# Kernel optimization log

Hardware: AMD Instinct MI355X
Metric: run time of the kernel (lower is better)

## Reference

```python
import jax, jax.numpy as jnp
import numpy as np

B, T1, T2, D, H = 16, 512, 64, 768, 12
E = D // H  # head dim


def _proj(x, W, b):
    # x: [B,T,D], W: [6,D,D], b: [6,D] -> [6,B,H,T,E], scaled by E**-0.25 (applied to q,k,v alike, per source)
    t = x.shape[1]
    p = jnp.einsum('btd,kdf->kbtf', x, W) + b[:, None, None, :]
    p = p.reshape(6, B, t, H, E).transpose(0, 1, 3, 2, 4)
    return p * (E ** -0.25)


def setup_inputs() -> dict:
    key = jax.random.key(0)
    ks = jax.random.split(key, 12)
    s = 0.02
    return {
        'feats': jax.random.normal(ks[0], (B, T1, D), jnp.float32),
        'inps': jax.random.normal(ks[1], (B, T2, D), jnp.float32),
        'att_mask': jax.random.randint(ks[2], (B, 1, 1, T1 + T2), 0, 2).astype(bool),
        'W_f': s * jax.random.normal(ks[3], (6, D, D), jnp.float32),
        'b_f': s * jax.random.normal(ks[4], (6, D), jnp.float32),
        'W_i': s * jax.random.normal(ks[5], (6, D, D), jnp.float32),
        'b_i': s * jax.random.normal(ks[6], (6, D), jnp.float32),
        'Wu_v': s * jax.random.normal(ks[7], (D, D), jnp.float32),
        'bu_v': s * jax.random.normal(ks[8], (D,), jnp.float32),
        'Wu_l': s * jax.random.normal(ks[9], (D, D), jnp.float32),
        'bu_l': s * jax.random.normal(ks[10], (D,), jnp.float32),
    }


def reference(feats, inps, att_mask, W_f, b_f, W_i, b_i, Wu_v, bu_v, Wu_l, bu_l):
    NEG = jnp.float32(-1e9)
    # projections from feats: [keys_v_v, queries_v_v, values_v_v, queries_l_v, keys_v_l, values_v_l]
    k_vv, q_vv, v_vv, q_lv, k_vl, v_vl = _proj(feats, W_f, b_f)
    # projections from inps: [keys_l_v, values_l_v, queries_v_l, queries_l_l, keys_l_l, values_l_l]
    k_lv, v_lv, q_vl, q_ll, k_ll, v_ll = _proj(inps, W_i, b_i)

    # visual stream: two distinct queries over the two key blocks, joint softmax over t1+t2
    dot_vv = jnp.einsum('bhqe,bhke->bhqk', q_vv, k_vv)   # [B,H,T1,T1]
    dot_lv = jnp.einsum('bhqe,bhke->bhqk', q_lv, k_lv)   # [B,H,T1,T2]
    att_v = jnp.concatenate([dot_vv, dot_lv], axis=-1)    # [B,H,T1,T1+T2]
    att_v = jax.nn.softmax(jnp.where(att_mask, NEG, att_v), axis=-1)
    vals_v = jnp.concatenate([v_vv, v_lv], axis=2)        # [B,H,T1+T2,E]
    out_v = jnp.einsum('bhqk,bhke->bhqe', att_v, vals_v)
    out_v = out_v.transpose(0, 2, 1, 3).reshape(B, T1, D)
    out_v = out_v @ Wu_v + bu_v

    # language stream
    dot_vl = jnp.einsum('bhqe,bhke->bhqk', q_vl, k_vl)    # [B,H,T2,T1]
    dot_ll = jnp.einsum('bhqe,bhke->bhqk', q_ll, k_ll)    # [B,H,T2,T2]
    att_l = jnp.concatenate([dot_vl, dot_ll], axis=-1)    # [B,H,T2,T1+T2]
    att_l = jax.nn.softmax(jnp.where(att_mask, NEG, att_l), axis=-1)
    vals_l = jnp.concatenate([v_vl, v_ll], axis=2)        # [B,H,T1+T2,E]
    out_l = jnp.einsum('bhqk,bhke->bhqe', att_l, vals_l)
    out_l = out_l.transpose(0, 2, 1, 3).reshape(B, T2, D)
    out_l = out_l @ Wu_l + bu_l

    return (out_v, out_l)
```

## Files before the change

### kernel.cpp

```cpp
#include <hip/hip_runtime.h>
#include <stdint.h>

#define BB 16
#define T1C 512
#define T2C 64
#define DC 768
#define HC 12
#define EC 64
#define SC 576
#define QSCALE 0.35355339059327379f

typedef __attribute__((ext_vector_type(8))) short bf16x8;
typedef __attribute__((ext_vector_type(4))) float f32x4;

__device__ __forceinline__ uint16_t f2b(float f) {
    union { float f; uint32_t i; } v; v.f = f;
    return (uint16_t)((v.i + 0x7fffu + ((v.i >> 16) & 1u)) >> 16);
}
__device__ __forceinline__ uint16_t f2bfast(float f) {
    union { float f; uint32_t i; } v; v.f = f;
    return (uint16_t)((v.i + 0x8000u) >> 16);
}
__device__ __forceinline__ uint32_t pk2(float a, float b) {
    return (uint32_t)f2b(a) | ((uint32_t)f2b(b) << 16);
}

__device__ __forceinline__ void gll16(const void* g, void* l) {
    __builtin_amdgcn_global_load_lds(
        (const __attribute__((address_space(1))) uint32_t*)(uintptr_t)g,
        (__attribute__((address_space(3))) uint32_t*)(uintptr_t)l, 16, 0, 0);
}

__global__ void detect(const uint32_t* __restrict__ mw, int* __restrict__ flags) {
    __shared__ int aW, aB, aL;
    if (threadIdx.x == 0) { aW = 0; aB = 0; aL = 0; }
    __syncthreads();
    int lW = 0, lB = 0, lL = 0;
    for (int i = threadIdx.x; i < 2304; i += 256) {
        uint32_t w = mw[i];
        if (w > 1u) lW = 1;
        if (((w) & 0xffu) > 1u || ((w >> 8) & 0xffu) > 1u ||
            ((w >> 16) & 0xffu) > 1u || ((w >> 24) & 0xffu) > 1u) lB = 1;
        if ((w & 0xffffu) > 1u) lL = 1;
    }
    if (lW) atomicOr(&aW, 1);
    if (lB) atomicOr(&aB, 1);
    if (lL) atomicOr(&aL, 1);
    __syncthreads();
    if (threadIdx.x == 0)
        flags[0] = (!aW) ? 0 : ((!aB) ? 1 : (aL ? 2 : 0));
}

__global__ __launch_bounds__(256) void wtrans(
    const float* __restrict__ Wf, const float* __restrict__ Wi,
    const float* __restrict__ Wuv, const float* __restrict__ Wul,
    uint16_t* __restrict__ Wt)
{
    __shared__ float tile[32][33];
    const int z = blockIdx.z;
    const float* src = (z < 6)  ? Wf + (size_t)z * DC * DC
                     : (z < 12) ? Wi + (size_t)(z - 6) * DC * DC
                     : (z == 12 ? Wuv : Wul);
    uint16_t* dst = Wt + (size_t)z * DC * DC;
    const int tx = threadIdx.x & 31, ty = threadIdx.x >> 5;
    const int k0 = blockIdx.x * 32, f0 = blockIdx.y * 32;
#pragma unroll
    for (int r = 0; r < 4; r++)
        tile[ty + r * 8][tx] = src[(size_t)(k0 + ty + r * 8) * DC + f0 + tx];
    __syncthreads();
#pragma unroll
    for (int r = 0; r < 4; r++)
        dst[(size_t)(f0 + ty + r * 8) * DC + k0 + tx] = f2b(tile[tx][ty + r * 8]);
}

__global__ __launch_bounds__(256) void xswz(
    const float* __restrict__ Xf, const float* __restrict__ Xi,
    uint16_t* __restrict__ Of, uint16_t* __restrict__ Oi)
{
    const int nf = BB * T1C * DC / 8;
    const int ni = BB * T2C * DC / 8;
    int t = blockIdx.x * 256 + threadIdx.x;
    const float* src; uint16_t* dst; int cc;
    if (t < nf) { src = Xf; dst = Of; cc = t; }
    else        { cc = t - nf; if (cc >= ni) return; src = Xi; dst = Oi; }
    int rlid = cc & 15;
    int t2 = cc >> 4;
    int qd = t2 & 3;
    int t3 = t2 >> 2;
    int kt = t3 % 24;
    int p  = t3 / 24;
    const float* sp = src + (size_t)(p * 16 + rlid) * DC + kt * 32 + qd * 8;
    float4 a = *(const float4*)sp;
    float4 b = *(const float4*)(sp + 4);
    uint4 o;
    o.x = pk2(a.x, a.y); o.y = pk2(a.z, a.w);
    o.z = pk2(b.x, b.y); o.w = pk2(b.z, b.w);
    *(uint4*)(dst + (size_t)cc * 8) = o;
}

#define BSTR 76

__global__ __launch_bounds__(256, 4) void gemm_proj_mfma(
    const uint16_t* __restrict__ Xsf, const uint16_t* __restrict__ Xsi,
    const uint16_t* __restrict__ Wt,
    const float* __restrict__ b_f, const float* __restrict__ b_i,
    uint16_t* __restrict__ Pf, uint16_t* __restrict__ Pi)
{
    __shared__ union {
        uint16_t B[2][128 * 32];
        uint16_t bounce[4][16 * BSTR];
    } sm;
    const int tid = threadIdx.x;
    const int w = tid >> 6, l = tid & 63;
    const bool isf = (blockIdx.x < 64);
    const int mx = isf ? blockIdx.x : blockIdx.x - 64;
    const int m0 = mx * 128;
    const int T  = isf ? T1C : T2C;
    const uint16_t* Xs = isf ? Xsf : Xsi;
    const float* bias  = isf ? b_f : b_i;
    uint16_t* P        = isf ? Pf : Pi;
    const int vmask    = isf ? 0x24 : 0x22;
    const int k6 = blockIdx.y / 6, nt = blockIdx.y % 6;
    const int n0 = nt * 128;
    const uint16_t* Bsrc = Wt + (size_t)((isf ? 0 : 6) + k6) * DC * DC;

    const int lid = l & 15, qd = l >> 4;
    const int wm = w >> 1, wn = w & 1;
    const int br = l >> 2, bk = (l & 3) * 8;
    const int p0 = mx * 8 + wm * 4;
    const int c0 = w * 2;

    f32x4 acc[4][4] = {};

#pragma unroll
    for (int n = 0; n < 2; ++n)
        gll16(Bsrc + (size_t)(n0 + (c0 + n) * 16 + br) * DC + bk, &sm.B[0][(c0 + n) * 512]);

    for (int kt = 0; kt < DC / 32; ++kt) {
        uint16_t* Bcur = sm.B[kt & 1];
        uint16_t* Bnxt = sm.B[(kt + 1) & 1];
        bf16x8 af[4];
#pragma unroll
        for (int i = 0; i < 4; i++)
            af[i] = *(const bf16x8*)(Xs + ((size_t)((p0 + i) * 24 + kt) * 64 + l) * 8);
        __builtin_amdgcn_s_barrier();
        __builtin_amdgcn_sched_barrier(0);
        if (kt < 23) {
#pragma unroll
            for (int n = 0; n < 2; ++n)
                gll16(Bsrc + (size_t)(n0 + (c0 + n) * 16 + br) * DC + (kt + 1) * 32 + bk,
                      &Bnxt[(c0 + n) * 512]);
            asm volatile("s_waitcnt vmcnt(2)" ::: "memory");
        } else {
            asm volatile("s_waitcnt vmcnt(0)" ::: "memory");
        }
        __builtin_amdgcn_sched_barrier(0);
        __builtin_amdgcn_s_barrier();
        __builtin_amdgcn_sched_barrier(0);
        bf16x8 bf[4];
#pragma unroll
        for (int j = 0; j < 4; j++)
            bf[j] = *(const bf16x8*)&Bcur[(wn * 64 + j * 16 + lid) * 32 + qd * 8];
#pragma unroll
        for (int i = 0; i < 4; i++)
#pragma unroll
            for (int j = 0; j < 4; j++)
                acc[i][j] = __builtin_amdgcn_mfma_f32_16x16x32_bf16(af[i], bf[j], acc[i][j], 0, 0, 0);
    }

    float bv[4];
#pragma unroll
    for (int j = 0; j < 4; j++)
        bv[j] = bias[k6 * DC + n0 + wn * 64 + j * 16 + lid];
    __syncthreads();

    uint16_t* reg = sm.bounce[w];
    const int mb = m0 + wm * 64;
    const int b = mb / T, tb = mb - b * T;
    const int h = nt * 2 + wn;
    const int rrow = l >> 2;
    const int rcol = (l & 3) * 16;

    if (!((vmask >> k6) & 1)) {
        uint16_t* dst0 = P + ((((size_t)k6 * BB + b) * HC + h) * T + tb + rrow) * EC + rcol;
#pragma unroll
        for (int p = 0; p < 4; p++) {
#pragma unroll
            for (int j = 0; j < 4; j++)
#pragma unroll
                for (int r = 0; r < 4; r++)
                    reg[(qd * 4 + r) * BSTR + j * 16 + lid] =
                        f2b((acc[p][j][r] + bv[j]) * QSCALE);
            uint4 d0 = *(const uint4*)&reg[rrow * BSTR + rcol];
            uint4 d1 = *(const uint4*)&reg[rrow * BSTR + rcol + 8];
            uint16_t* dst = dst0 + (size_t)p * 16 * EC;
            *(uint4*)dst = d0;
            *(uint4*)(dst + 8) = d1;
        }
    } else {
        uint16_t* dst0 = P + (size_t)k6 * BB * HC * T * EC
                           + (((size_t)b * HC + h) * EC + rrow) * T + tb + rcol;
#pragma unroll
        for (int p = 0; p < 4; p++) {
#pragma unroll
            for (int i = 0; i < 4; i++) {
                uint32_t w0 = pk2((acc[i][p][0] + bv[p]) * QSCALE,
                                  (acc[i][p][1] + bv[p]) * QSCALE);
                uint32_t w1 = pk2((acc[i][p][2] + bv[p]) * QSCALE,
                                  (acc[i][p][3] + bv[p]) * QSCALE);
                *(uint2*)&reg[lid * BSTR + i * 16 + qd * 4] = make_uint2(w0, w1);
            }
            uint4 d0 = *(const uint4*)&reg[rrow * BSTR + rcol];
            uint4 d1 = *(const uint4*)&reg[rrow * BSTR + rcol + 8];
            uint16_t* dst = dst0 + (size_t)p * 16 * T;
            *(uint4*)dst = d0;
            *(uint4*)(dst + 8) = d1;
        }
    }
}

__global__ __launch_bounds__(256, 4) void gemm_out_mfma(
    const uint16_t* __restrict__ Osv, const uint16_t* __restrict__ Osl,
    const uint16_t* __restrict__ Wt,
    const float* __restrict__ bu_v, const float* __restrict__ bu_l,
    float* __restrict__ out)
{
    __shared__ uint16_t Bs[2][128 * 32];
    const int tid = threadIdx.x;
    const int w = tid >> 6, l = tid & 63;
    const bool isv = (blockIdx.x < 64);
    const int mx = isv ? blockIdx.x : blockIdx.x - 64;
    const int m0 = mx * 128;
    const int rowoff = isv ? 0 : BB * T1C;
    const uint16_t* A = isv ? Osv : Osl;
    const uint16_t* Wtm = Wt + (size_t)(isv ? 12 : 13) * DC * DC;
    const float* bias = isv ? bu_v : bu_l;
    const int n0 = blockIdx.y * 128;
    const int lid = l & 15, qd = l >> 4;
    const int wm = w >> 1, wn = w & 1;
    const int br = l >> 2, bk = (l & 3) * 8;
    const int p0 = mx * 8 + wm * 4;
    const int c0 = w * 2;

    f32x4 acc[4][4] = {};

#pragma unroll
    for (int n = 0; n < 2; ++n)
        gll16(Wtm + (size_t)(n0 + (c0 + n) * 16 + br) * DC + bk, &Bs[0][(c0 + n) * 512]);

    for (int kt = 0; kt < DC / 32; ++kt) {
        uint16_t* Bcur = Bs[kt & 1];
        uint16_t* Bnxt = Bs[(kt + 1) & 1];
        bf16x8 af[4];
#pragma unroll
        for (int i = 0; i < 4; i++)
            af[i] = *(const bf16x8*)(A + ((size_t)((p0 + i) * 24 + kt) * 64 + l) * 8);
        __builtin_amdgcn_s_barrier();
        __builtin_amdgcn_sched_barrier(0);
        if (kt < 23) {
#pragma unroll
            for (int n = 0; n < 2; ++n)
                gll16(Wtm + (size_t)(n0 + (c0 + n) * 16 + br) * DC + (kt + 1) * 32 + bk,
                      &Bnxt[(c0 + n) * 512]);
            asm volatile("s_waitcnt vmcnt(2)" ::: "memory");
        } else {
            asm volatile("s_waitcnt vmcnt(0)" ::: "memory");
        }
        __builtin_amdgcn_sched_barrier(0);
        __builtin_amdgcn_s_barrier();
        __builtin_amdgcn_sched_barrier(0);
        bf16x8 bf[4];
#pragma unroll
        for (int j = 0; j < 4; j++)
            bf[j] = *(const bf16x8*)&Bcur[(wn * 64 + j * 16 + lid) * 32 + qd * 8];
#pragma unroll
        for (int i = 0; i < 4; i++)
#pragma unroll
            for (int j = 0; j < 4; j++)
                acc[i][j] = __builtin_amdgcn_mfma_f32_16x16x32_bf16(af[i], bf[j], acc[i][j], 0, 0, 0);
    }

    float bv[4];
#pragma unroll
    for (int j = 0; j < 4; j++)
        bv[j] = bias[n0 + wn * 64 + j * 16 + lid];
#pragma unroll
    for (int i = 0; i < 4; i++)
#pragma unroll
        for (int j = 0; j < 4; j++)
#pragma unroll
            for (int r = 0; r < 4; r++) {
                int m = m0 + wm * 64 + i * 16 + qd * 4 + r;
                int f = n0 + wn * 64 + j * 16 + lid;
                out[(size_t)(rowoff + m) * DC + f] = acc[i][j][r] + bv[j];
            }
}

__global__ __launch_bounds__(256, 3) void attn_mfma(
    const uint16_t* __restrict__ Pf,
    const uint16_t* __restrict__ Pi,
    const void* __restrict__ maskp,
    const int* __restrict__ flags,
    uint16_t* __restrict__ Osv,
    uint16_t* __restrict__ Osl)
{
    __shared__ uint16_t Klds[64 * 72];
    __shared__ uint16_t Vlds[64 * 72];
    __shared__ uint16_t Plds[4][16 * 72];
    __shared__ float    Ma[SC];
    __shared__ float    Lw[4][16];

    const int bh = blockIdx.x;
    const int tile = blockIdx.y;
    const int b = bh / HC, h = bh % HC;
    const int tid = threadIdx.x;
    const int w = tid >> 6, l = tid & 63;
    const int lid = l & 15, qd = l >> 4;

    const size_t SF = (size_t)BB * HC * T1C * EC;
    const size_t SI = (size_t)BB * HC * T2C * EC;

    const bool vis = (tile < 8);
    const uint16_t *Qa, *Qb, *K1, *K2, *V1, *V2;
    uint16_t* O; int Tq, q0;
    if (vis) { Qa = Pf + 1 * SF; Qb = Pf + 3 * SF; K1 = Pf;          K2 = Pi;
               V1 = Pf + 2 * SF; V2 = Pi + 1 * SI; O = Osv; Tq = T1C; q0 = tile * 64; }
    else     { Qa = Pi + 2 * SI; Qb = Pi + 3 * SI; K1 = Pf + 4 * SF; K2 = Pi + 4 * SI;
               V1 = Pf + 5 * SF; V2 = Pi + 5 * SI; O = Osl; Tq = T2C; q0 = 0; }

    {
        const int kind = flags[0];
        for (int i = tid; i < SC; i += 256) {
            int idx = b * SC + i;
            int mv;
            if (kind == 0)      mv = ((const uint32_t*)maskp)[idx] != 0u;
            else if (kind == 1) mv = ((const uint8_t*)maskp)[idx] != 0;
            else                mv = ((const uint16_t*)maskp)[idx] != 0;
            Ma[i] = mv ? -1e9f : 0.0f;
        }
    }

    const int q = q0 + w * 16 + lid;
    const uint16_t* Qrow  = Qa + ((size_t)bh * Tq + q) * EC;
    const uint16_t* Qrow2 = Qb + ((size_t)bh * Tq + q) * EC;
    bf16x8 qf0 = *(const bf16x8*)(Qrow + qd * 8);
    bf16x8 qf1 = *(const bf16x8*)(Qrow + 32 + qd * 8);
    bf16x8 qg0 = *(const bf16x8*)(Qrow2 + qd * 8);
    bf16x8 qg1 = *(const bf16x8*)(Qrow2 + 32 + qd * 8);

    f32x4 o[4];
#pragma unroll
    for (int ef = 0; ef < 4; ef++) { o[ef][0]=0.f; o[ef][1]=0.f; o[ef][2]=0.f; o[ef][3]=0.f; }
    float u[4] = {0.f, 0.f, 0.f, 0.f};

    const int skey = tid >> 2, se0 = (tid & 3) * 16;
    const int ve = tid >> 2,  vc = tid & 3;

    auto kptr = [&](int c) -> const uint16_t* {
        return (c < 8) ? K1 + ((size_t)bh * T1C + c * 64 + skey) * EC + se0
                       : K2 + ((size_t)bh * T2C + skey) * EC + se0;
    };
    auto vptr = [&](int c) -> const uint16_t* {
        return (c < 8) ? V1 + ((size_t)bh * EC + ve) * T1C + c * 64 + vc * 16
                       : V2 + ((size_t)bh * EC + ve) * T2C + vc * 16;
    };

    uint4 ka0 = *(const uint4*)kptr(0);
    uint4 ka1 = *(const uint4*)(kptr(0) + 8);
    uint4 va0 = *(const uint4*)vptr(0);
    uint4 va1 = *(const uint4*)(vptr(0) + 8);

#pragma unroll
    for (int c = 0; c < 9; ++c) {
        uint4 kb0, kb1, vb0, vb1;
        if (c < 8) {
            kb0 = *(const uint4*)kptr(c + 1);
            kb1 = *(const uint4*)(kptr(c + 1) + 8);
            vb0 = *(const uint4*)vptr(c + 1);
            vb1 = *(const uint4*)(vptr(c + 1) + 8);
        }
        __builtin_amdgcn_s_barrier();
        __builtin_amdgcn_sched_barrier(0);
        *(uint4*)&Klds[skey * 72 + se0]         = ka0;
        *(uint4*)&Klds[skey * 72 + se0 + 8]     = ka1;
        *(uint4*)&Vlds[ve * 72 + vc * 16]       = va0;
        *(uint4*)&Vlds[ve * 72 + vc * 16 + 8]   = va1;
        asm volatile("s_waitcnt lgkmcnt(0)" ::: "memory");
        __builtin_amdgcn_sched_barrier(0);
        __builtin_amdgcn_s_barrier();
        __builtin_amdgcn_sched_barrier(0);

        const int k0 = c * 64;
        const bf16x8 q_0 = (c < 8) ? qf0 : qg0;
        const bf16x8 q_1 = (c < 8) ? qf1 : qg1;
        f32x4 s[4];
#pragma unroll
        for (int sub = 0; sub < 4; sub++) {
            bf16x8 kf0 = *(const bf16x8*)&Klds[(sub * 16 + lid) * 72 + qd * 8];
            bf16x8 kf1 = *(const bf16x8*)&Klds[(sub * 16 + lid) * 72 + 32 + qd * 8];
            f32x4 z; z[0]=0.f; z[1]=0.f; z[2]=0.f; z[3]=0.f;
            z = __builtin_amdgcn_mfma_f32_16x16x32_bf16(q_0, kf0, z, 0, 0, 0);
            s[sub] = __builtin_amdgcn_mfma_f32_16x16x32_bf16(q_1, kf1, z, 0, 0, 0);
        }
#pragma unroll
        for (int sub = 0; sub < 4; sub++) {
            float mv = Ma[k0 + sub * 16 + lid];
#pragma unroll
            for (int r = 0; r < 4; r++) {
                float p = __expf(s[sub][r] + mv);
                u[r] += p;
                Plds[w][(qd * 4 + r) * 72 + sub * 16 + lid] = f2bfast(p);
            }
        }
#pragma unroll
        for (int half = 0; half < 2; half++) {
            bf16x8 pf = *(const bf16x8*)&Plds[w][lid * 72 + half * 32 + qd * 8];
#pragma unroll
            for (int ef = 0; ef < 4; ef++) {
                bf16x8 vf = *(const bf16x8*)&Vlds[(ef * 16 + lid) * 72 + half * 32 + qd * 8];
                o[ef] = __builtin_amdgcn_mfma_f32_16x16x32_bf16(vf, pf, o[ef], 0, 0, 0);
            }
        }
        if (c < 8) { ka0 = kb0; ka1 = kb1; va0 = vb0; va1 = vb1; }
    }

#pragma unroll
    for (int d = 1; d <= 8; d <<= 1)
#pragma unroll
        for (int r = 0; r < 4; r++)
            u[r] += __shfl_xor(u[r], d, 64);
    if (lid == 0) {
#pragma unroll
        for (int r = 0; r < 4; r++) Lw[w][qd * 4 + r] = u[r];
    }
    float rl = 1.f / Lw[w][lid];

    const size_t p = ((size_t)b * Tq + q0 + w * 16) >> 4;
#pragma unroll
    for (int ef = 0; ef < 4; ef++) {
        uint32_t w0 = pk2(o[ef][0] * rl, o[ef][1] * rl);
        uint32_t w1 = pk2(o[ef][2] * rl, o[ef][3] * rl);
        size_t chunk = ((p * 24 + h * 2 + (ef >> 1)) * 4 + (ef & 1) * 2 + (qd >> 1)) * 16 + lid;
        *(uint2*)(O + chunk * 8 + (qd & 1) * 4) = make_uint2(w0, w1);
    }
}

extern "C" void kernel_launch(void* const* d_in, const int* in_sizes, int n_in,
                              void* d_out, int out_size, void* d_ws, size_t ws_size,
                              hipStream_t stream)
{
    const float* feats = (const float*)d_in[0];
    const float* inps  = (const float*)d_in[1];
    const void*  maskp = d_in[2];
    const float* W_f   = (const float*)d_in[3];
    const float* b_f   = (const float*)d_in[4];
    const float* W_i   = (const float*)d_in[5];
    const float* b_i   = (const float*)d_in[6];
    const float* Wu_v  = (const float*)d_in[7];
    const float* bu_v  = (const float*)d_in[8];
    const float* Wu_l  = (const float*)d_in[9];
    const float* bu_l  = (const float*)d_in[10];

    const size_t MAT = (size_t)DC * DC;
    const size_t PF_E = 6ull * BB * HC * T1C * EC;
    const size_t PI_E = 6ull * BB * HC * T2C * EC;
    uint16_t* Wt  = (uint16_t*)d_ws;
    uint16_t* Osv = Wt;
    uint16_t* Osl = Wt + (size_t)BB * T1C * HC * EC;
    uint16_t* Pf  = Wt + 14 * MAT;
    uint16_t* Pi  = Pf + PF_E;
    int* flags    = (int*)(Pi + PI_E);

    uint16_t* Xsf = (uint16_t*)d_out;
    uint16_t* Xsi = Xsf + (size_t)BB * T1C * DC;

    detect<<<dim3(1), dim3(256), 0, stream>>>((const uint32_t*)maskp, flags);

    wtrans<<<dim3(24, 24, 14), dim3(256), 0, stream>>>(W_f, W_i, Wu_v, Wu_l, Wt);

    {
        int nchunks = (BB * T1C * DC + BB * T2C * DC) / 8;
        xswz<<<dim3((nchunks + 255) / 256), dim3(256), 0, stream>>>(feats, inps, Xsf, Xsi);
    }

    gemm_proj_mfma<<<dim3(72, 36), dim3(256), 0, stream>>>(
        Xsf, Xsi, Wt, b_f, b_i, Pf, Pi);

    attn_mfma<<<dim3(BB * HC, 9), dim3(256), 0, stream>>>(
        Pf, Pi, maskp, flags, Osv, Osl);

    gemm_out_mfma<<<dim3(72, 6), dim3(256), 0, stream>>>(
        Osv, Osl, Wt, bu_v, bu_l, (float*)d_out);
}
```

Measured before the change: 264.4 us.

## Merge prep kernels and double-buffer A-fragment loads in both GEMMs

Folds the mask detection, weight transpose and input swizzle kernels into one launch dispatched by block index, removing two kernel launches and their gaps. Both MFMA GEMMs now unroll the K loop by two and keep two sets of A fragments in registers, so the global loads for the next K step are issued before the current step's MFMAs and their latency is hidden. Occupancy hints drop from 4 to 3 blocks per CU to make room for the extra registers, which may reduce latency hiding across waves.

```diff
diff --git a/kernel.cpp b/kernel.cpp
--- a/kernel.cpp
+++ b/kernel.cpp
@@ -31,76 +31,78 @@
         (__attribute__((address_space(3))) uint32_t*)(uintptr_t)l, 16, 0, 0);
 }
 
-__global__ void detect(const uint32_t* __restrict__ mw, int* __restrict__ flags) {
-    __shared__ int aW, aB, aL;
-    if (threadIdx.x == 0) { aW = 0; aB = 0; aL = 0; }
-    __syncthreads();
-    int lW = 0, lB = 0, lL = 0;
-    for (int i = threadIdx.x; i < 2304; i += 256) {
-        uint32_t w = mw[i];
-        if (w > 1u) lW = 1;
-        if (((w) & 0xffu) > 1u || ((w >> 8) & 0xffu) > 1u ||
-            ((w >> 16) & 0xffu) > 1u || ((w >> 24) & 0xffu) > 1u) lB = 1;
-        if ((w & 0xffffu) > 1u) lL = 1;
-    }
-    if (lW) atomicOr(&aW, 1);
-    if (lB) atomicOr(&aB, 1);
-    if (lL) atomicOr(&aL, 1);
-    __syncthreads();
-    if (threadIdx.x == 0)
-        flags[0] = (!aW) ? 0 : ((!aB) ? 1 : (aL ? 2 : 0));
-}
-
-__global__ __launch_bounds__(256) void wtrans(
+#define WT_BLOCKS (24 * 24 * 14)
+#define XS_BLOCKS 3456
+
+__global__ __launch_bounds__(256) void prep(
     const float* __restrict__ Wf, const float* __restrict__ Wi,
     const float* __restrict__ Wuv, const float* __restrict__ Wul,
-    uint16_t* __restrict__ Wt)
+    uint16_t* __restrict__ Wt,
+    const float* __restrict__ Xf, const float* __restrict__ Xi,
+    uint16_t* __restrict__ Of, uint16_t* __restrict__ Oi,
+    const uint32_t* __restrict__ mw, int* __restrict__ flags)
 {
-    __shared__ float tile[32][33];
-    const int z = blockIdx.z;
-    const float* src = (z < 6)  ? Wf + (size_t)z * DC * DC
-                     : (z < 12) ? Wi + (size_t)(z - 6) * DC * DC
-                     : (z == 12 ? Wuv : Wul);
-    uint16_t* dst = Wt + (size_t)z * DC * DC;
-    const int tx = threadIdx.x & 31, ty = threadIdx.x >> 5;
-    const int k0 = blockIdx.x * 32, f0 = blockIdx.y * 32;
-#pragma unroll
-    for (int r = 0; r < 4; r++)
-        tile[ty + r * 8][tx] = src[(size_t)(k0 + ty + r * 8) * DC + f0 + tx];
-    __syncthreads();
-#pragma unroll
-    for (int r = 0; r < 4; r++)
-        dst[(size_t)(f0 + ty + r * 8) * DC + k0 + tx] = f2b(tile[tx][ty + r * 8]);
-}
-
-__global__ __launch_bounds__(256) void xswz(
-    const float* __restrict__ Xf, const float* __restrict__ Xi,
-    uint16_t* __restrict__ Of, uint16_t* __restrict__ Oi)
-{
-    const int nf = BB * T1C * DC / 8;
-    const int ni = BB * T2C * DC / 8;
-    int t = blockIdx.x * 256 + threadIdx.x;
-    const float* src; uint16_t* dst; int cc;
-    if (t < nf) { src = Xf; dst = Of; cc = t; }
-    else        { cc = t - nf; if (cc >= ni) return; src = Xi; dst = Oi; }
-    int rlid = cc & 15;
-    int t2 = cc >> 4;
-    int qd = t2 & 3;
-    int t3 = t2 >> 2;
-    int kt = t3 % 24;
-    int p  = t3 / 24;
-    const float* sp = src + (size_t)(p * 16 + rlid) * DC + kt * 32 + qd * 8;
-    float4 a = *(const float4*)sp;
-    float4 b = *(const float4*)(sp + 4);
-    uint4 o;
-    o.x = pk2(a.x, a.y); o.y = pk2(a.z, a.w);
-    o.z = pk2(b.x, b.y); o.w = pk2(b.z, b.w);
-    *(uint4*)(dst + (size_t)cc * 8) = o;
+    __shared__ union { float tile[32][33]; int d[3]; } sh;
+    const int bid = blockIdx.x;
+    if (bid < WT_BLOCKS) {
+        const int z = bid / 576, r = bid % 576;
+        const int kx = r % 24, fy = r / 24;
+        const float* src = (z < 6)  ? Wf + (size_t)z * DC * DC
+                         : (z < 12) ? Wi + (size_t)(z - 6) * DC * DC
+                         : (z == 12 ? Wuv : Wul);
+        uint16_t* dst = Wt + (size_t)z * DC * DC;
+        const int tx = threadIdx.x & 31, ty = threadIdx.x >> 5;
+        const int k0 = kx * 32, f0 = fy * 32;
+#pragma unroll
+        for (int q = 0; q < 4; q++)
+            sh.tile[ty + q * 8][tx] = src[(size_t)(k0 + ty + q * 8) * DC + f0 + tx];
+        __syncthreads();
+#pragma unroll
+        for (int q = 0; q < 4; q++)
+            dst[(size_t)(f0 + ty + q * 8) * DC + k0 + tx] = f2b(sh.tile[tx][ty + q * 8]);
+    } else if (bid < WT_BLOCKS + XS_BLOCKS) {
+        const int nf = BB * T1C * DC / 8;
+        const int ni = BB * T2C * DC / 8;
+        int t = (bid - WT_BLOCKS) * 256 + threadIdx.x;
+        const float* src; uint16_t* dst; int cc;
+        if (t < nf) { src = Xf; dst = Of; cc = t; }
+        else        { cc = t - nf; if (cc >= ni) return; src = Xi; dst = Oi; }
+        int rlid = cc & 15;
+        int t2 = cc >> 4;
+        int qd = t2 & 3;
+        int t3 = t2 >> 2;
+        int kt = t3 % 24;
+        int p  = t3 / 24;
+        const float* sp = src + (size_t)(p * 16 + rlid) * DC + kt * 32 + qd * 8;
+        float4 a = *(const float4*)sp;
+        float4 b = *(const float4*)(sp + 4);
+        uint4 o;
+        o.x = pk2(a.x, a.y); o.y = pk2(a.z, a.w);
+        o.z = pk2(b.x, b.y); o.w = pk2(b.z, b.w);
+        *(uint4*)(dst + (size_t)cc * 8) = o;
+    } else {
+        if (threadIdx.x == 0) { sh.d[0] = 0; sh.d[1] = 0; sh.d[2] = 0; }
+        __syncthreads();
+        int lW = 0, lB = 0, lL = 0;
+        for (int i = threadIdx.x; i < 2304; i += 256) {
+            uint32_t w = mw[i];
+            if (w > 1u) lW = 1;
+            if (((w) & 0xffu) > 1u || ((w >> 8) & 0xffu) > 1u ||
+                ((w >> 16) & 0xffu) > 1u || ((w >> 24) & 0xffu) > 1u) lB = 1;
+            if ((w & 0xffffu) > 1u) lL = 1;
+        }
+        if (lW) atomicOr(&sh.d[0], 1);
+        if (lB) atomicOr(&sh.d[1], 1);
+        if (lL) atomicOr(&sh.d[2], 1);
+        __syncthreads();
+        if (threadIdx.x == 0)
+            flags[0] = (!sh.d[0]) ? 0 : ((!sh.d[1]) ? 1 : (sh.d[2] ? 2 : 0));
+    }
 }
 
 #define BSTR 76
 
-__global__ __launch_bounds__(256, 4) void gemm_proj_mfma(
+__global__ __launch_bounds__(256, 3) void gemm_proj_mfma(
     const uint16_t* __restrict__ Xsf, const uint16_t* __restrict__ Xsi,
     const uint16_t* __restrict__ Wt,
     const float* __restrict__ b_f, const float* __restrict__ b_i,
@@ -131,42 +133,50 @@
     const int c0 = w * 2;
 
     f32x4 acc[4][4] = {};
-
-#pragma unroll
-    for (int n = 0; n < 2; ++n)
-        gll16(Bsrc + (size_t)(n0 + (c0 + n) * 16 + br) * DC + bk, &sm.B[0][(c0 + n) * 512]);
-
-    for (int kt = 0; kt < DC / 32; ++kt) {
-        uint16_t* Bcur = sm.B[kt & 1];
-        uint16_t* Bnxt = sm.B[(kt + 1) & 1];
-        bf16x8 af[4];
-#pragma unroll
-        for (int i = 0; i < 4; i++)
-            af[i] = *(const bf16x8*)(Xs + ((size_t)((p0 + i) * 24 + kt) * 64 + l) * 8);
-        __builtin_amdgcn_s_barrier();
-        __builtin_amdgcn_sched_barrier(0);
-        if (kt < 23) {
-#pragma unroll
-            for (int n = 0; n < 2; ++n)
-                gll16(Bsrc + (size_t)(n0 + (c0 + n) * 16 + br) * DC + (kt + 1) * 32 + bk,
-                      &Bnxt[(c0 + n) * 512]);
-            asm volatile("s_waitcnt vmcnt(2)" ::: "memory");
+    bf16x8 af0[4], af1[4];
+
+#define PJ_A(dst, t) { _Pragma("unroll") for (int i = 0; i < 4; i++) \
+        dst[i] = *(const bf16x8*)(Xs + ((size_t)((p0 + i) * 24 + (t)) * 64 + l) * 8); }
+#define PJ_S(bu, t) { _Pragma("unroll") for (int n = 0; n < 2; n++) \
+        gll16(Bsrc + (size_t)(n0 + (c0 + n) * 16 + br) * DC + (t) * 32 + bk, \
+              &sm.B[bu][(c0 + n) * 512]); }
+#define PJ_C(bu, afc) { bf16x8 bq[4]; \
+        _Pragma("unroll") for (int j = 0; j < 4; j++) \
+            bq[j] = *(const bf16x8*)&sm.B[bu][(wn * 64 + j * 16 + lid) * 32 + qd * 8]; \
+        _Pragma("unroll") for (int i = 0; i < 4; i++) \
+        _Pragma("unroll") for (int j = 0; j < 4; j++) \
+            acc[i][j] = __builtin_amdgcn_mfma_f32_16x16x32_bf16(afc[i], bq[j], acc[i][j], 0, 0, 0); }
+
+    PJ_A(af0, 0);
+    PJ_S(0, 0);
+
+    for (int k2 = 0; k2 < 12; ++k2) {
+        PJ_A(af1, 2 * k2 + 1);
+        __builtin_amdgcn_s_barrier();
+        __builtin_amdgcn_sched_barrier(0);
+        PJ_S(1, 2 * k2 + 1);
+        asm volatile("s_waitcnt vmcnt(6)" ::: "memory");
+        __builtin_amdgcn_sched_barrier(0);
+        __builtin_amdgcn_s_barrier();
+        __builtin_amdgcn_sched_barrier(0);
+        PJ_C(0, af0);
+        if (k2 < 11) { PJ_A(af0, 2 * k2 + 2); }
+        __builtin_amdgcn_s_barrier();
+        __builtin_amdgcn_sched_barrier(0);
+        if (k2 < 11) {
+            PJ_S(0, 2 * k2 + 2);
+            asm volatile("s_waitcnt vmcnt(6)" ::: "memory");
         } else {
             asm volatile("s_waitcnt vmcnt(0)" ::: "memory");
         }
         __builtin_amdgcn_sched_barrier(0);
         __builtin_amdgcn_s_barrier();
         __builtin_amdgcn_sched_barrier(0);
-        bf16x8 bf[4];
-#pragma unroll
-        for (int j = 0; j < 4; j++)
-            bf[j] = *(const bf16x8*)&Bcur[(wn * 64 + j * 16 + lid) * 32 + qd * 8];
-#pragma unroll
-        for (int i = 0; i < 4; i++)
-#pragma unroll
-            for (int j = 0; j < 4; j++)
-                acc[i][j] = __builtin_amdgcn_mfma_f32_16x16x32_bf16(af[i], bf[j], acc[i][j], 0, 0, 0);
-    }
+        PJ_C(1, af1);
+    }
+#undef PJ_A
+#undef PJ_S
+#undef PJ_C
 
     float bv[4];
 #pragma unroll
@@ -219,7 +229,7 @@
     }
 }
 
-__global__ __launch_bounds__(256, 4) void gemm_out_mfma(
+__global__ __launch_bounds__(256, 3) void gemm_out_mfma(
     const uint16_t* __restrict__ Osv, const uint16_t* __restrict__ Osl,
     const uint16_t* __restrict__ Wt,
     const float* __restrict__ bu_v, const float* __restrict__ bu_l,
@@ -243,42 +253,50 @@
     const int c0 = w * 2;
 
     f32x4 acc[4][4] = {};
-
-#pragma unroll
-    for (int n = 0; n < 2; ++n)
-        gll16(Wtm + (size_t)(n0 + (c0 + n) * 16 + br) * DC + bk, &Bs[0][(c0 + n) * 512]);
-
-    for (int kt = 0; kt < DC / 32; ++kt) {
-        uint16_t* Bcur = Bs[kt & 1];
-        uint16_t* Bnxt = Bs[(kt + 1) & 1];
-        bf16x8 af[4];
-#pragma unroll
-        for (int i = 0; i < 4; i++)
-            af[i] = *(const bf16x8*)(A + ((size_t)((p0 + i) * 24 + kt) * 64 + l) * 8);
-        __builtin_amdgcn_s_barrier();
-        __builtin_amdgcn_sched_barrier(0);
-        if (kt < 23) {
-#pragma unroll
-            for (int n = 0; n < 2; ++n)
-                gll16(Wtm + (size_t)(n0 + (c0 + n) * 16 + br) * DC + (kt + 1) * 32 + bk,
-                      &Bnxt[(c0 + n) * 512]);
-            asm volatile("s_waitcnt vmcnt(2)" ::: "memory");
+    bf16x8 af0[4], af1[4];
+
+#define GO_A(dst, t) { _Pragma("unroll") for (int i = 0; i < 4; i++) \
+        dst[i] = *(const bf16x8*)(A + ((size_t)((p0 + i) * 24 + (t)) * 64 + l) * 8); }
+#define GO_S(bu, t) { _Pragma("unroll") for (int n = 0; n < 2; n++) \
+        gll16(Wtm + (size_t)(n0 + (c0 + n) * 16 + br) * DC + (t) * 32 + bk, \
+              &Bs[bu][(c0 + n) * 512]); }
+#define GO_C(bu, afc) { bf16x8 bq[4]; \
+        _Pragma("unroll") for (int j = 0; j < 4; j++) \
+            bq[j] = *(const bf16x8*)&Bs[bu][(wn * 64 + j * 16 + lid) * 32 + qd * 8]; \
+        _Pragma("unroll") for (int i = 0; i < 4; i++) \
+        _Pragma("unroll") for (int j = 0; j < 4; j++) \
+            acc[i][j] = __builtin_amdgcn_mfma_f32_16x16x32_bf16(afc[i], bq[j], acc[i][j], 0, 0, 0); }
+
+    GO_A(af0, 0);
+    GO_S(0, 0);
+
+    for (int k2 = 0; k2 < 12; ++k2) {
+        GO_A(af1, 2 * k2 + 1);
+        __builtin_amdgcn_s_barrier();
+        __builtin_amdgcn_sched_barrier(0);
+        GO_S(1, 2 * k2 + 1);
+        asm volatile("s_waitcnt vmcnt(6)" ::: "memory");
+        __builtin_amdgcn_sched_barrier(0);
+        __builtin_amdgcn_s_barrier();
+        __builtin_amdgcn_sched_barrier(0);
+        GO_C(0, af0);
+        if (k2 < 11) { GO_A(af0, 2 * k2 + 2); }
+        __builtin_amdgcn_s_barrier();
+        __builtin_amdgcn_sched_barrier(0);
+        if (k2 < 11) {
+            GO_S(0, 2 * k2 + 2);
+            asm volatile("s_waitcnt vmcnt(6)" ::: "memory");
         } else {
             asm volatile("s_waitcnt vmcnt(0)" ::: "memory");
         }
         __builtin_amdgcn_sched_barrier(0);
         __builtin_amdgcn_s_barrier();
         __builtin_amdgcn_sched_barrier(0);
-        bf16x8 bf[4];
-#pragma unroll
-        for (int j = 0; j < 4; j++)
-            bf[j] = *(const bf16x8*)&Bcur[(wn * 64 + j * 16 + lid) * 32 + qd * 8];
-#pragma unroll
-        for (int i = 0; i < 4; i++)
-#pragma unroll
-            for (int j = 0; j < 4; j++)
-                acc[i][j] = __builtin_amdgcn_mfma_f32_16x16x32_bf16(af[i], bf[j], acc[i][j], 0, 0, 0);
-    }
+        GO_C(1, af1);
+    }
+#undef GO_A
+#undef GO_S
+#undef GO_C
 
     float bv[4];
 #pragma unroll
@@ -474,14 +492,9 @@
     uint16_t* Xsf = (uint16_t*)d_out;
     uint16_t* Xsi = Xsf + (size_t)BB * T1C * DC;
 
-    detect<<<dim3(1), dim3(256), 0, stream>>>((const uint32_t*)maskp, flags);
-
-    wtrans<<<dim3(24, 24, 14), dim3(256), 0, stream>>>(W_f, W_i, Wu_v, Wu_l, Wt);
-
-    {
-        int nchunks = (BB * T1C * DC + BB * T2C * DC) / 8;
-        xswz<<<dim3((nchunks + 255) / 256), dim3(256), 0, stream>>>(feats, inps, Xsf, Xsi);
-    }
+    prep<<<dim3(WT_BLOCKS + XS_BLOCKS + 1), dim3(256), 0, stream>>>(
+        W_f, W_i, Wu_v, Wu_l, Wt, feats, inps, Xsf, Xsi,
+        (const uint32_t*)maskp, flags);
 
     gemm_proj_mfma<<<dim3(72, 36), dim3(256), 0, stream>>>(
         Xsf, Xsi, Wt, b_f, b_i, Pf, Pi);
```

After: 257.1 us. 2.7% less time.
